# Kernel optimization log

Measured on AMD Instinct MI355X. Metric: run time of the kernel, lower is better.

## Reference

```python
import jax, jax.numpy as jnp
import numpy as np

N, E = 50000, 1600000
F_IN, EDGE_DIM, HID, HEADS, NCLS = 64, 16, 128, 4, 40
C = HID // HEADS  # per-head dim = 32


def setup_inputs() -> dict:
    key = jax.random.key(0)
    ks = jax.random.split(key, 20)
    s = 0.1
    inp = {
        'x': jax.random.normal(ks[0], (N, F_IN), jnp.float32),
        'edge_index': jax.random.randint(ks[1], (2, E), 0, N, jnp.int64),
        'edge_attr': jax.random.normal(ks[2], (E, EDGE_DIM), jnp.float32),
        # layer 1 params
        'W1': jax.random.normal(ks[3], (HID, F_IN), jnp.float32) * s,
        'as1': jax.random.normal(ks[4], (HEADS, C), jnp.float32) * s,
        'ad1': jax.random.normal(ks[5], (HEADS, C), jnp.float32) * s,
        'ae1': jax.random.normal(ks[6], (HEADS, C), jnp.float32) * s,
        'We1': jax.random.normal(ks[7], (HID, EDGE_DIM), jnp.float32) * s,
        'b1': jnp.zeros((HID,), jnp.float32),
        # layer 2 params
        'W2': jax.random.normal(ks[8], (HID, HID), jnp.float32) * s,
        'as2': jax.random.normal(ks[9], (HEADS, C), jnp.float32) * s,
        'ad2': jax.random.normal(ks[10], (HEADS, C), jnp.float32) * s,
        'ae2': jax.random.normal(ks[11], (HEADS, C), jnp.float32) * s,
        'We2': jax.random.normal(ks[12], (HID, EDGE_DIM), jnp.float32) * s,
        'b2': jnp.zeros((HID,), jnp.float32),
        # final classifier
        'Wlin': jax.random.normal(ks[13], (NCLS, HID), jnp.float32) * s,
        'blin': jnp.zeros((NCLS,), jnp.float32),
    }
    return inp


def gat_conv(x, src, dst, eattr, W, a_s, a_d, a_e, We, b):
    """PyG GATConv (concat=True, add_self_loops=True, fill_value='mean'), eval mode."""
    n = x.shape[0]
    H, Cd = a_s.shape
    h = (x @ W.T).reshape(n, H, Cd)  # [N,H,C]
    # self-loop edge_attr = per-destination mean of incoming edge_attr
    cnt = jax.ops.segment_sum(jnp.ones((dst.shape[0],), eattr.dtype), dst, num_segments=n)
    mean_ea = jax.ops.segment_sum(eattr, dst, num_segments=n) / jnp.maximum(cnt, 1.0)[:, None]
    loops = jnp.arange(n, dtype=src.dtype)
    s_idx = jnp.concatenate([src, loops])
    d_idx = jnp.concatenate([dst, loops])
    ea = jnp.concatenate([eattr, mean_ea], axis=0)  # [E+N, edge_dim]
    e = (ea @ We.T).reshape(-1, H, Cd)
    # edge-wise attention logits
    alpha = (h * a_s).sum(-1)[s_idx] + (h * a_d).sum(-1)[d_idx] + (e * a_e).sum(-1)  # [E+N,H]
    alpha = jax.nn.leaky_relu(alpha, 0.2)
    # segment softmax over destination neighborhoods (every node has a self-loop)
    amax = jax.ops.segment_max(alpha, d_idx, num_segments=n)
    ex = jnp.exp(alpha - amax[d_idx])
    den = jax.ops.segment_sum(ex, d_idx, num_segments=n)
    coef = ex / (den[d_idx] + 1e-16)
    out = jax.ops.segment_sum(h[s_idx] * coef[:, :, None], d_idx, num_segments=n)
    return out.reshape(n, H * Cd) + b


def reference(x, edge_index, edge_attr, W1, as1, ad1, ae1, We1, b1,
              W2, as2, ad2, ae2, We2, b2, Wlin, blin):
    src, dst = edge_index[0], edge_index[1]
    h = jax.nn.relu(gat_conv(x, src, dst, edge_attr, W1, as1, ad1, ae1, We1, b1))
    h = jax.nn.relu(gat_conv(h, src, dst, edge_attr, W2, as2, ad2, ae2, We2, b2))
    logits = h @ Wlin.T + blin
    return jax.nn.log_softmax(logits, axis=1)
```

## Files before the change

kernel.cpp:

```cpp
#include <hip/hip_runtime.h>
#include <hip/hip_bf16.h>
#include <math.h>


#define CHUNK 8192
#define CAPC 12288

typedef __attribute__((ext_vector_type(8))) short short8;
typedef __attribute__((ext_vector_type(4))) float floatx4;

__device__ __forceinline__ unsigned short f2bf(float f) {
  unsigned u = __float_as_uint(f);
  unsigned r = u + 0x7FFFu + ((u >> 16) & 1u);
  return (unsigned short)(r >> 16);
}
__device__ __forceinline__ float bf2f(unsigned short b) {
  return __uint_as_float(((unsigned)b) << 16);
}

__global__ __launch_bounds__(512) void hist_kernel(const int* __restrict__ dst,
                                                   int* __restrict__ bucketCnt,
                                                   int E, int NB) {
  __shared__ int hist[512];
  const int tid = threadIdx.x;
  hist[tid] = 0;
  __syncthreads();
  const int e0 = blockIdx.x * CHUNK, e1 = min(e0 + CHUNK, E);
  for (int e = e0 + tid; e < e1; e += 512) atomicAdd(&hist[dst[e] >> 7], 1);
  __syncthreads();
  if (tid < NB && hist[tid]) atomicAdd(&bucketCnt[tid], hist[tid]);
}

__global__ __launch_bounds__(512) void scanB_kernel(const int* __restrict__ bucketCnt,
                                                    int* __restrict__ bucketOffs,
                                                    int* __restrict__ bucketPos,
                                                    int* __restrict__ offs,
                                                    int NB, int N, int E) {
  __shared__ int sc[512];
  const int tid = threadIdx.x;
  const int v = (tid < NB) ? bucketCnt[tid] : 0;
  sc[tid] = v;
  __syncthreads();
  for (int off = 1; off < 512; off <<= 1) {
    int t = (tid >= off) ? sc[tid - off] : 0;
    __syncthreads();
    sc[tid] += t;
    __syncthreads();
  }
  const int excl = sc[tid] - v;
  if (tid < NB) { bucketOffs[tid] = excl; bucketPos[tid] = excl; }
  if (tid == 0) { bucketOffs[NB] = E; offs[N] = E; }
}

__global__ __launch_bounds__(512) void partB_kernel(const int* __restrict__ src,
                                                    const int* __restrict__ dst,
                                                    int* __restrict__ bucketPos,
                                                    int2* __restrict__ binned,
                                                    int E, int NB) {
  __shared__ int hist[512], sc[512], lbase[513], gbase[512], lcnt[512];
  __shared__ int2 stage[CHUNK];
  const int tid = threadIdx.x;
  const int e0 = blockIdx.x * CHUNK;
  const int e1 = min(e0 + CHUNK, E);
  hist[tid] = 0; lcnt[tid] = 0;
  __syncthreads();
  for (int e = e0 + tid; e < e1; e += 512) atomicAdd(&hist[dst[e] >> 7], 1);
  __syncthreads();
  sc[tid] = hist[tid];
  __syncthreads();
  for (int off = 1; off < 512; off <<= 1) {
    int t = (tid >= off) ? sc[tid - off] : 0;
    __syncthreads();
    sc[tid] += t;
    __syncthreads();
  }
  lbase[tid + 1] = sc[tid];
  if (tid == 0) lbase[0] = 0;
  if (tid < NB && hist[tid] > 0) gbase[tid] = atomicAdd(&bucketPos[tid], hist[tid]);
  __syncthreads();
  for (int e = e0 + tid; e < e1; e += 512) {
    const int d = dst[e];
    const int b = d >> 7;
    const int lr = atomicAdd(&lcnt[b], 1);
    int2 v;
    v.x = src[e];
    v.y = (int)(((unsigned)(d & 127) << 25) | (unsigned)e);
    stage[lbase[b] + lr] = v;
  }
  __syncthreads();
  const int total = e1 - e0;
  for (int t = tid; t < total; t += 512) {
    int lo = 0, hi = 511;
    while (lo < hi) {
      int mid = (lo + hi + 1) >> 1;
      if (lbase[mid] <= t) lo = mid; else hi = mid - 1;
    }
    binned[gbase[lo] + (t - lbase[lo])] = stage[t];
  }
}

__global__ __launch_bounds__(256) void passC_kernel(const int2* __restrict__ binned,
                                                    const int* __restrict__ bucketOffs,
                                                    int* __restrict__ srcS,
                                                    int* __restrict__ elist,
                                                    int* __restrict__ offs, int N) {
  __shared__ int cnt[128], dbase[129], dpos[128];
  __shared__ int2 stage[CAPC];
  const int tid = threadIdx.x;
  const int b = blockIdx.x;
  const int bo = bucketOffs[b], be = bucketOffs[b + 1];
  const int m = be - bo;
  if (tid < 128) { cnt[tid] = 0; dpos[tid] = 0; }
  __syncthreads();
  for (int t = tid; t < m; t += 256) {
    int2 v = binned[bo + t];
    if (t < CAPC) stage[t] = v;
    atomicAdd(&cnt[((unsigned)v.y) >> 25], 1);
  }
  __syncthreads();
  for (int off = 1; off < 128; off <<= 1) {
    int t = (tid < 128 && tid >= (unsigned)off) ? cnt[tid - off] : 0;
    __syncthreads();
    if (tid < 128) cnt[tid] += t;
    __syncthreads();
  }
  if (tid == 0) dbase[0] = 0;
  if (tid < 128) dbase[tid + 1] = cnt[tid];
  __syncthreads();
  const int dcnt = min(128, N - (b << 7));
  if (tid < dcnt) offs[(b << 7) + tid] = bo + dbase[tid];
  for (int t = tid; t < m; t += 256) {
    int2 v = (t < CAPC) ? stage[t] : binned[bo + t];
    const unsigned py = (unsigned)v.y;
    const int dl = py >> 25;
    const int p = dbase[dl] + atomicAdd(&dpos[dl], 1);
    srcS[bo + p] = v.x;
    elist[bo + p] = (int)(py & 0x1FFFFFFu);
  }
}

__global__ __launch_bounds__(128) void wa_kernel(const float* __restrict__ ae1,
                                                 const float* __restrict__ We1,
                                                 const float* __restrict__ ae2,
                                                 const float* __restrict__ We2,
                                                 float* __restrict__ Wa) {
  int t = threadIdx.x;
  const float* ae = (t < 64) ? ae1 : ae2;
  const float* We = (t < 64) ? We1 : We2;
  int h = (t >> 4) & 3;
  int d = t & 15;
  float s = 0.f;
  for (int c = 0; c < 32; ++c) s += ae[h * 32 + c] * We[(h * 32 + c) * 16 + d];
  Wa[t] = s;
}

__global__ __launch_bounds__(256) void cvt3_kernel(const float* __restrict__ a,
                                                   unsigned short* __restrict__ ao, int na,
                                                   const float* __restrict__ b,
                                                   unsigned short* __restrict__ bo, int nb,
                                                   const float* __restrict__ c,
                                                   unsigned short* __restrict__ co, int nc) {
  int i = blockIdx.x * 256 + threadIdx.x;
  if (i < na) ao[i] = f2bf(a[i]);
  else if (i < na + nb) bo[i - na] = f2bf(b[i - na]);
  else if (i < na + nb + nc) co[i - na - nb] = f2bf(c[i - na - nb]);
}

__global__ __launch_bounds__(256) void cvtw_kernel(const float* __restrict__ Wlin,
                                                   unsigned short* __restrict__ whi,
                                                   unsigned short* __restrict__ wlo) {
  int i = blockIdx.x * 256 + threadIdx.x;
  if (i >= 48 * 128) return;
  float v = (i < 40 * 128) ? Wlin[i] : 0.f;
  unsigned short h = f2bf(v);
  whi[i] = h;
  wlo[i] = f2bf(v - bf2f(h));
}

__global__ __launch_bounds__(256) void alphae12_kernel(const int* __restrict__ elist,
                                                       const float* __restrict__ ea,
                                                       const float* __restrict__ Wa,
                                                       unsigned short* __restrict__ ae1s,
                                                       unsigned short* __restrict__ ae2s,
                                                       int E) {
  __shared__ float wa[128];
  if (threadIdx.x < 128) wa[threadIdx.x] = Wa[threadIdx.x];
  __syncthreads();
  int j = blockIdx.x * 256 + threadIdx.x;
  if (j >= E) return;
  const int e = elist[j];
  const float4* p = (const float4*)(ea + (size_t)e * 16);
  float4 q0 = p[0], q1 = p[1], q2 = p[2], q3 = p[3];
  float v[16] = {q0.x, q0.y, q0.z, q0.w, q1.x, q1.y, q1.z, q1.w,
                 q2.x, q2.y, q2.z, q2.w, q3.x, q3.y, q3.z, q3.w};
  unsigned short rr[8];
#pragma unroll
  for (int h = 0; h < 8; ++h) {
    float s = 0.f;
#pragma unroll
    for (int d = 0; d < 16; ++d) s += v[d] * wa[h * 16 + d];
    rr[h] = f2bf(s);
  }
  ushort4 lo; lo.x = rr[0]; lo.y = rr[1]; lo.z = rr[2]; lo.w = rr[3];
  ushort4 hi; hi.x = rr[4]; hi.y = rr[5]; hi.z = rr[6]; hi.w = rr[7];
  *(ushort4*)(ae1s + (size_t)j * 4) = lo;
  *(ushort4*)(ae2s + (size_t)j * 4) = hi;
}

__global__ __launch_bounds__(256) void gemm_mfma_kernel(const unsigned short* __restrict__ X,
                                                        const unsigned short* __restrict__ Wb,
                                                        unsigned short* __restrict__ H,
                                                        int n, int K) {
  const int w = threadIdx.x >> 6;
  const int lane = threadIdx.x & 63;
  const int m0 = blockIdx.x * 64;
  const int quad = lane >> 4;
  const int l15 = lane & 15;
  floatx4 acc[4][2];
#pragma unroll
  for (int mt = 0; mt < 4; ++mt)
#pragma unroll
    for (int nt = 0; nt < 2; ++nt) acc[mt][nt] = (floatx4)(0.f);

  int rowm[4];
#pragma unroll
  for (int mt = 0; mt < 4; ++mt) {
    int r = m0 + mt * 16 + l15;
    rowm[mt] = (r < n) ? r : (n - 1);
  }
  const int ncol0 = (w << 5) + l15;

  for (int kc = 0; kc < K; kc += 32) {
    const int koff = kc + (quad << 3);
    short8 a[4], b[2];
#pragma unroll
    for (int mt = 0; mt < 4; ++mt)
      a[mt] = *(const short8*)(X + (size_t)rowm[mt] * K + koff);
#pragma unroll
    for (int nt = 0; nt < 2; ++nt)
      b[nt] = *(const short8*)(Wb + (size_t)(ncol0 + nt * 16) * K + koff);
#pragma unroll
    for (int mt = 0; mt < 4; ++mt)
#pragma unroll
      for (int nt = 0; nt < 2; ++nt)
        acc[mt][nt] = __builtin_amdgcn_mfma_f32_16x16x32_bf16(a[mt], b[nt], acc[mt][nt], 0, 0, 0);
  }
#pragma unroll
  for (int mt = 0; mt < 4; ++mt) {
    const int rbase = m0 + mt * 16 + (quad << 2);
#pragma unroll
    for (int nt = 0; nt < 2; ++nt) {
      const int col = ncol0 + nt * 16;
#pragma unroll
      for (int r = 0; r < 4; ++r) {
        const int row = rbase + r;
        if (row < n) H[(size_t)row * 128 + col] = f2bf(acc[mt][nt][r]);
      }
    }
  }
}

__global__ __launch_bounds__(256) void score_kernel(const unsigned short* __restrict__ h,
                                                    const float* __restrict__ a_s,
                                                    const float* __restrict__ a_d,
                                                    float* __restrict__ ssc,
                                                    float* __restrict__ dsc, int n) {
  int gid = blockIdx.x * 256 + threadIdx.x;
  int node = gid >> 6;
  int lane = threadIdx.x & 63;
  if (node >= n) return;
  int ch = lane * 2;
  ushort2 hq = *(const ushort2*)(h + (size_t)node * 128 + ch);
  float h0 = bf2f(hq.x), h1 = bf2f(hq.y);
  float ps = h0 * a_s[ch] + h1 * a_s[ch + 1];
  float pd = h0 * a_d[ch] + h1 * a_d[ch + 1];
#pragma unroll
  for (int off = 8; off; off >>= 1) {
    ps += __shfl_xor(ps, off, 16);
    pd += __shfl_xor(pd, off, 16);
  }
  if ((lane & 15) == 0) {
    int head = lane >> 4;
    ssc[node * 4 + head] = ps;
    dsc[node * 4 + head] = pd;
  }
}

__device__ __forceinline__ float leaky02(float a) { return a > 0.f ? a : 0.2f * a; }
__device__ __forceinline__ float sel4(float4 v, int h) {
  return (h == 0) ? v.x : (h == 1) ? v.y : (h == 2) ? v.z : v.w;
}

__global__ __launch_bounds__(256) void agg_kernel(const unsigned short* __restrict__ hin,
                                                  const float* __restrict__ ssc,
                                                  const float* __restrict__ dsc,
                                                  const unsigned short* __restrict__ aeS,
                                                  const int* __restrict__ offs,
                                                  const int* __restrict__ srcS,
                                                  const float* __restrict__ bias,
                                                  unsigned short* __restrict__ hout, int n) {
  __shared__ int sbuf[4][64];
  __shared__ float pbuf[4][256];
  const int tid = threadIdx.x;
  const int wv = tid >> 6;
  const int lane = tid & 63;
  const int node = blockIdx.x * 4 + wv;
  if (node >= n) return;
  const int l32 = lane & 31;
  const int half = lane >> 5;
  const int ch4 = l32 * 4;
  const int headB = l32 >> 3;
  const float4 dv = *(const float4*)(dsc + (size_t)node * 4);
  float4 l4 = make_float4(0.f, 0.f, 0.f, 0.f);
  float4 sa = make_float4(0.f, 0.f, 0.f, 0.f);
  float acc[4] = {0.f, 0.f, 0.f, 0.f};
  const int j0 = offs[node], j1 = offs[node + 1];

  for (int jc = j0; jc < j1; jc += 64) {
    const int len = min(64, j1 - jc);
    float4 p4 = make_float4(0.f, 0.f, 0.f, 0.f);
    int sv = 0;
    if (lane < len) {
      const int j = jc + lane;
      sv = srcS[j];
      const ushort4 aq = *(const ushort4*)(aeS + (size_t)j * 4);
      const float4 ae4 = make_float4(bf2f(aq.x), bf2f(aq.y), bf2f(aq.z), bf2f(aq.w));
      const float4 ss4 = *(const float4*)(ssc + (size_t)sv * 4);
      sa.x += ae4.x; sa.y += ae4.y; sa.z += ae4.z; sa.w += ae4.w;
      p4.x = __expf(leaky02(ss4.x + dv.x + ae4.x));
      p4.y = __expf(leaky02(ss4.y + dv.y + ae4.y));
      p4.z = __expf(leaky02(ss4.z + dv.z + ae4.z));
      p4.w = __expf(leaky02(ss4.w + dv.w + ae4.w));
    }
    sbuf[wv][lane] = sv;
    *(float4*)(&pbuf[wv][lane * 4]) = p4;
    l4.x += p4.x; l4.y += p4.y; l4.z += p4.z; l4.w += p4.w;
    int k = 0;
    for (; k + 8 <= len; k += 8) {
      int kk0 = k + half, kk1 = k + 2 + half, kk2 = k + 4 + half, kk3 = k + 6 + half;
      int s0 = sbuf[wv][kk0], s1 = sbuf[wv][kk1], s2 = sbuf[wv][kk2], s3 = sbuf[wv][kk3];
      float p0 = pbuf[wv][kk0 * 4 + headB], p1 = pbuf[wv][kk1 * 4 + headB];
      float p2 = pbuf[wv][kk2 * 4 + headB], p3 = pbuf[wv][kk3 * 4 + headB];
      uint2 d0 = *(const uint2*)(hin + (size_t)s0 * 128 + ch4);
      uint2 d1 = *(const uint2*)(hin + (size_t)s1 * 128 + ch4);
      uint2 d2 = *(const uint2*)(hin + (size_t)s2 * 128 + ch4);
      uint2 d3 = *(const uint2*)(hin + (size_t)s3 * 128 + ch4);
      acc[0] += p0 * __uint_as_float(d0.x << 16);
      acc[1] += p0 * __uint_as_float(d0.x & 0xFFFF0000u);
      acc[2] += p0 * __uint_as_float(d0.y << 16);
      acc[3] += p0 * __uint_as_float(d0.y & 0xFFFF0000u);
      acc[0] += p1 * __uint_as_float(d1.x << 16);
      acc[1] += p1 * __uint_as_float(d1.x & 0xFFFF0000u);
      acc[2] += p1 * __uint_as_float(d1.y << 16);
      acc[3] += p1 * __uint_as_float(d1.y & 0xFFFF0000u);
      acc[0] += p2 * __uint_as_float(d2.x << 16);
      acc[1] += p2 * __uint_as_float(d2.x & 0xFFFF0000u);
      acc[2] += p2 * __uint_as_float(d2.y << 16);
      acc[3] += p2 * __uint_as_float(d2.y & 0xFFFF0000u);
      acc[0] += p3 * __uint_as_float(d3.x << 16);
      acc[1] += p3 * __uint_as_float(d3.x & 0xFFFF0000u);
      acc[2] += p3 * __uint_as_float(d3.y << 16);
      acc[3] += p3 * __uint_as_float(d3.y & 0xFFFF0000u);
    }
    for (; k < len; k += 2) {
      int kk = k + half;
      if (kk < len) {
        int s = sbuf[wv][kk];
        float p = pbuf[wv][kk * 4 + headB];
        uint2 d = *(const uint2*)(hin + (size_t)s * 128 + ch4);
        acc[0] += p * __uint_as_float(d.x << 16);
        acc[1] += p * __uint_as_float(d.x & 0xFFFF0000u);
        acc[2] += p * __uint_as_float(d.y << 16);
        acc[3] += p * __uint_as_float(d.y & 0xFFFF0000u);
      }
    }
  }

#pragma unroll
  for (int off = 32; off; off >>= 1) {
    sa.x += __shfl_xor(sa.x, off);
    sa.y += __shfl_xor(sa.y, off);
    sa.z += __shfl_xor(sa.z, off);
    sa.w += __shfl_xor(sa.w, off);
    l4.x += __shfl_xor(l4.x, off);
    l4.y += __shfl_xor(l4.y, off);
    l4.z += __shfl_xor(l4.z, off);
    l4.w += __shfl_xor(l4.w, off);
  }
#pragma unroll
  for (int i = 0; i < 4; ++i) acc[i] += __shfl_xor(acc[i], 32);

  const int deg = j1 - j0;
  const float invd = 1.f / fmaxf((float)deg, 1.f);
  const float ssn = ssc[(size_t)node * 4 + headB];
  const float aloop = leaky02(ssn + sel4(dv, headB) + sel4(sa, headB) * invd);
  const float pl = __expf(aloop);
  const float lF = sel4(l4, headB) + pl;
  const uint2 hd = *(const uint2*)(hin + (size_t)node * 128 + ch4);
  const float hv0 = __uint_as_float(hd.x << 16);
  const float hv1 = __uint_as_float(hd.x & 0xFFFF0000u);
  const float hv2 = __uint_as_float(hd.y << 16);
  const float hv3 = __uint_as_float(hd.y & 0xFFFF0000u);
  const float inv = 1.f / (lF + 1e-16f);
  const float4 bi = *(const float4*)(bias + ch4);
  const float o0 = fmaxf((acc[0] + pl * hv0) * inv + bi.x, 0.f);
  const float o1 = fmaxf((acc[1] + pl * hv1) * inv + bi.y, 0.f);
  const float o2 = fmaxf((acc[2] + pl * hv2) * inv + bi.z, 0.f);
  const float o3 = fmaxf((acc[3] + pl * hv3) * inv + bi.w, 0.f);
  if (half == 0) {
    ushort4 o;
    o.x = f2bf(o0); o.y = f2bf(o1); o.z = f2bf(o2); o.w = f2bf(o3);
    *(ushort4*)(hout + (size_t)node * 128 + ch4) = o;
  }
}

__global__ __launch_bounds__(256) void classifier_kernel(const unsigned short* __restrict__ h,
                                                         const unsigned short* __restrict__ Whi,
                                                         const unsigned short* __restrict__ Wlo,
                                                         const float* __restrict__ blin,
                                                         float* __restrict__ out, int n) {
  const int w = threadIdx.x >> 6;
  const int lane = threadIdx.x & 63;
  const int quad = lane >> 4;
  const int l15 = lane & 15;
  const int row0 = blockIdx.x * 64 + w * 16;
  if (row0 >= n) return;
  int rowm = row0 + l15;
  if (rowm >= n) rowm = n - 1;
  floatx4 acc[3];
#pragma unroll
  for (int nt = 0; nt < 3; ++nt) acc[nt] = (floatx4)(0.f);
  const size_t hbase = (size_t)rowm * 128;
#pragma unroll
  for (int kc = 0; kc < 128; kc += 32) {
    const int koff = kc + (quad << 3);
    short8 a = *(const short8*)(h + hbase + koff);
#pragma unroll
    for (int nt = 0; nt < 3; ++nt) {
      short8 bh = *(const short8*)(Whi + (size_t)(nt * 16 + l15) * 128 + koff);
      short8 bl = *(const short8*)(Wlo + (size_t)(nt * 16 + l15) * 128 + koff);
      acc[nt] = __builtin_amdgcn_mfma_f32_16x16x32_bf16(a, bh, acc[nt], 0, 0, 0);
      acc[nt] = __builtin_amdgcn_mfma_f32_16x16x32_bf16(a, bl, acc[nt], 0, 0, 0);
    }
  }
  const float bl0 = blin[l15];
  const float bl1 = blin[16 + l15];
  const float bl2 = (l15 < 8) ? blin[32 + l15] : 0.f;
#pragma unroll
  for (int r = 0; r < 4; ++r) {
    const int rrow = row0 + (quad << 2) + r;
    const float v0 = acc[0][r] + bl0;
    const float v1 = acc[1][r] + bl1;
    const float v2 = (l15 < 8) ? (acc[2][r] + bl2) : -INFINITY;
    float m = fmaxf(v0, fmaxf(v1, v2));
#pragma unroll
    for (int off = 8; off; off >>= 1) m = fmaxf(m, __shfl_xor(m, off, 16));
    const float e2 = (l15 < 8) ? __expf(v2 - m) : 0.f;
    float s = __expf(v0 - m) + __expf(v1 - m) + e2;
#pragma unroll
    for (int off = 8; off; off >>= 1) s += __shfl_xor(s, off, 16);
    const float ls = m + __logf(s);
    if (rrow < n) {
      float* po = out + (size_t)rrow * 40;
      po[l15] = v0 - ls;
      po[16 + l15] = v1 - ls;
      if (l15 < 8) po[32 + l15] = v2 - ls;
    }
  }
}

extern "C" void kernel_launch(void* const* d_in, const int* in_sizes, int n_in,
                              void* d_out, int out_size, void* d_ws, size_t ws_size,
                              hipStream_t stream) {
  const float* x    = (const float*)d_in[0];
  const int*   eidx = (const int*)d_in[1];
  const float* ea   = (const float*)d_in[2];
  const float* W1   = (const float*)d_in[3];
  const float* as1  = (const float*)d_in[4];
  const float* ad1  = (const float*)d_in[5];
  const float* ae1w = (const float*)d_in[6];
  const float* We1  = (const float*)d_in[7];
  const float* b1   = (const float*)d_in[8];
  const float* W2   = (const float*)d_in[9];
  const float* as2  = (const float*)d_in[10];
  const float* ad2  = (const float*)d_in[11];
  const float* ae2w = (const float*)d_in[12];
  const float* We2  = (const float*)d_in[13];
  const float* b2   = (const float*)d_in[14];
  const float* Wlin = (const float*)d_in[15];
  const float* blin = (const float*)d_in[16];
  float* out = (float*)d_out;

  const int N = in_sizes[0] / 64;
  const int E = in_sizes[1] / 2;
  const int* src = eidx;
  const int* dst = eidx + E;
  const int NB = (N + 127) >> 7;

  char* wsb = (char*)d_ws;
  size_t off = 0;
  auto alloc = [&](size_t bytes) -> void* {
    void* p = wsb + off;
    off = (off + bytes + 255) & ~(size_t)255;
    return p;
  };
  int* bucketCnt  = (int*)alloc(512 * 4);
  int* bucketOffs = (int*)alloc(513 * 4);
  int* bucketPos  = (int*)alloc(512 * 4);
  int* offs       = (int*)alloc((size_t)(N + 1) * 4);
  void* bhA       = alloc((size_t)E * 8 > (size_t)N * 256 ? (size_t)E * 8 : (size_t)N * 256);
  int2* binned    = (int2*)bhA;
  unsigned short* hA = (unsigned short*)bhA;
  int* srcS       = (int*)alloc((size_t)E * 4);
  int* elist      = (int*)alloc((size_t)E * 4);
  float* Wa       = (float*)alloc(128 * 4);
  unsigned short* xb  = (unsigned short*)alloc((size_t)N * 64 * 2);
  unsigned short* Wb1 = (unsigned short*)alloc(128 * 64 * 2);
  unsigned short* Wb2 = (unsigned short*)alloc(128 * 128 * 2);
  unsigned short* Wlh = (unsigned short*)alloc(48 * 128 * 2);
  unsigned short* Wll = (unsigned short*)alloc(48 * 128 * 2);
  float* ssc      = (float*)alloc((size_t)N * 4 * 4);
  float* dsc      = (float*)alloc((size_t)N * 4 * 4);
  unsigned short* ae1s = (unsigned short*)alloc((size_t)E * 4 * 2);
  unsigned short* ae2s = (unsigned short*)alloc((size_t)E * 4 * 2);
  unsigned short* hB   = (unsigned short*)alloc((size_t)N * 128 * 2);

  const int ge = (E + 255) / 256;
  const int gg = (N + 63) / 64;
  const int gn = (N + 3) / 4;
  const int gp = (E + CHUNK - 1) / CHUNK;
  const int ncvt = N * 64 + 128 * 64 + 128 * 128;

  hipMemsetAsync(bucketCnt, 0, 512 * 4, stream);
  hist_kernel<<<gp, 512, 0, stream>>>(dst, bucketCnt, E, NB);
  scanB_kernel<<<1, 512, 0, stream>>>(bucketCnt, bucketOffs, bucketPos, offs, NB, N, E);
  partB_kernel<<<gp, 512, 0, stream>>>(src, dst, bucketPos, binned, E, NB);
  passC_kernel<<<NB, 256, 0, stream>>>(binned, bucketOffs, srcS, elist, offs, N);

  wa_kernel<<<1, 128, 0, stream>>>(ae1w, We1, ae2w, We2, Wa);
  cvt3_kernel<<<(ncvt + 255) / 256, 256, 0, stream>>>(x, xb, N * 64, W1, Wb1, 128 * 64,
                                                      W2, Wb2, 128 * 128);
  cvtw_kernel<<<24, 256, 0, stream>>>(Wlin, Wlh, Wll);
  alphae12_kernel<<<ge, 256, 0, stream>>>(elist, ea, Wa, ae1s, ae2s, E);

  gemm_mfma_kernel<<<gg, 256, 0, stream>>>(xb, Wb1, hA, N, 64);
  score_kernel<<<gn, 256, 0, stream>>>(hA, as1, ad1, ssc, dsc, N);
  agg_kernel<<<gn, 256, 0, stream>>>(hA, ssc, dsc, ae1s, offs, srcS, b1, hB, N);

  gemm_mfma_kernel<<<gg, 256, 0, stream>>>(hB, Wb2, hA, N, 128);
  score_kernel<<<gn, 256, 0, stream>>>(hA, as2, ad2, ssc, dsc, N);
  agg_kernel<<<gn, 256, 0, stream>>>(hA, ssc, dsc, ae2s, offs, srcS, b2, hB, N);

  classifier_kernel<<<gg, 256, 0, stream>>>(hB, Wlh, Wll, blin, out, N);
}
```

Before: 483.8 us.

## Map one aggregation node per half-wave with 8-deep unrolled neighbor gathers

The GAT aggregation kernel now assigns each destination node to 32 lanes instead of a full 64-lane wave, so each block covers 8 nodes. Edges are processed in 32-wide chunks, and the gather loop is unrolled 8-deep with all loads issued before any accumulation. This is meant to cut idle lanes for average-degree nodes, remove the cross-half accumulator reduction, and keep more memory loads in flight. The self-feature and bias loads are hoisted to the start of the kernel. In exchange, two nodes with different degrees now share one wave, which can cause loop divergence, and register pressure rises.

```diff
diff --git a/kernel.cpp b/kernel.cpp
--- a/kernel.cpp
+++ b/kernel.cpp
@@ -299,29 +299,29 @@
                                                   const int* __restrict__ srcS,
                                                   const float* __restrict__ bias,
                                                   unsigned short* __restrict__ hout, int n) {
-  __shared__ int sbuf[4][64];
-  __shared__ float pbuf[4][256];
+  __shared__ int sbuf[8][32];
+  __shared__ float pbuf[8][128];
   const int tid = threadIdx.x;
-  const int wv = tid >> 6;
-  const int lane = tid & 63;
-  const int node = blockIdx.x * 4 + wv;
+  const int hw = tid >> 5;
+  const int l32 = tid & 31;
+  const int node = blockIdx.x * 8 + hw;
   if (node >= n) return;
-  const int l32 = lane & 31;
-  const int half = lane >> 5;
   const int ch4 = l32 * 4;
   const int headB = l32 >> 3;
   const float4 dv = *(const float4*)(dsc + (size_t)node * 4);
+  const uint2 hd = *(const uint2*)(hin + (size_t)node * 128 + ch4);
+  const float4 bi = *(const float4*)(bias + ch4);
   float4 l4 = make_float4(0.f, 0.f, 0.f, 0.f);
   float4 sa = make_float4(0.f, 0.f, 0.f, 0.f);
   float acc[4] = {0.f, 0.f, 0.f, 0.f};
   const int j0 = offs[node], j1 = offs[node + 1];
 
-  for (int jc = j0; jc < j1; jc += 64) {
-    const int len = min(64, j1 - jc);
+  for (int jc = j0; jc < j1; jc += 32) {
+    const int len = min(32, j1 - jc);
     float4 p4 = make_float4(0.f, 0.f, 0.f, 0.f);
     int sv = 0;
-    if (lane < len) {
-      const int j = jc + lane;
+    if (l32 < len) {
+      const int j = jc + l32;
       sv = srcS[j];
       const ushort4 aq = *(const ushort4*)(aeS + (size_t)j * 4);
       const float4 ae4 = make_float4(bf2f(aq.x), bf2f(aq.y), bf2f(aq.z), bf2f(aq.w));
@@ -332,52 +332,44 @@
       p4.z = __expf(leaky02(ss4.z + dv.z + ae4.z));
       p4.w = __expf(leaky02(ss4.w + dv.w + ae4.w));
     }
-    sbuf[wv][lane] = sv;
-    *(float4*)(&pbuf[wv][lane * 4]) = p4;
+    sbuf[hw][l32] = sv;
+    *(float4*)(&pbuf[hw][l32 * 4]) = p4;
     l4.x += p4.x; l4.y += p4.y; l4.z += p4.z; l4.w += p4.w;
+
     int k = 0;
     for (; k + 8 <= len; k += 8) {
-      int kk0 = k + half, kk1 = k + 2 + half, kk2 = k + 4 + half, kk3 = k + 6 + half;
-      int s0 = sbuf[wv][kk0], s1 = sbuf[wv][kk1], s2 = sbuf[wv][kk2], s3 = sbuf[wv][kk3];
-      float p0 = pbuf[wv][kk0 * 4 + headB], p1 = pbuf[wv][kk1 * 4 + headB];
-      float p2 = pbuf[wv][kk2 * 4 + headB], p3 = pbuf[wv][kk3 * 4 + headB];
-      uint2 d0 = *(const uint2*)(hin + (size_t)s0 * 128 + ch4);
-      uint2 d1 = *(const uint2*)(hin + (size_t)s1 * 128 + ch4);
-      uint2 d2 = *(const uint2*)(hin + (size_t)s2 * 128 + ch4);
-      uint2 d3 = *(const uint2*)(hin + (size_t)s3 * 128 + ch4);
-      acc[0] += p0 * __uint_as_float(d0.x << 16);
-      acc[1] += p0 * __uint_as_float(d0.x & 0xFFFF0000u);
-      acc[2] += p0 * __uint_as_float(d0.y << 16);
-      acc[3] += p0 * __uint_as_float(d0.y & 0xFFFF0000u);
-      acc[0] += p1 * __uint_as_float(d1.x << 16);
-      acc[1] += p1 * __uint_as_float(d1.x & 0xFFFF0000u);
-      acc[2] += p1 * __uint_as_float(d1.y << 16);
-      acc[3] += p1 * __uint_as_float(d1.y & 0xFFFF0000u);
-      acc[0] += p2 * __uint_as_float(d2.x << 16);
-      acc[1] += p2 * __uint_as_float(d2.x & 0xFFFF0000u);
-      acc[2] += p2 * __uint_as_float(d2.y << 16);
-      acc[3] += p2 * __uint_as_float(d2.y & 0xFFFF0000u);
-      acc[0] += p3 * __uint_as_float(d3.x << 16);
-      acc[1] += p3 * __uint_as_float(d3.x & 0xFFFF0000u);
-      acc[2] += p3 * __uint_as_float(d3.y << 16);
-      acc[3] += p3 * __uint_as_float(d3.y & 0xFFFF0000u);
-    }
-    for (; k < len; k += 2) {
-      int kk = k + half;
-      if (kk < len) {
-        int s = sbuf[wv][kk];
-        float p = pbuf[wv][kk * 4 + headB];
-        uint2 d = *(const uint2*)(hin + (size_t)s * 128 + ch4);
-        acc[0] += p * __uint_as_float(d.x << 16);
-        acc[1] += p * __uint_as_float(d.x & 0xFFFF0000u);
-        acc[2] += p * __uint_as_float(d.y << 16);
-        acc[3] += p * __uint_as_float(d.y & 0xFFFF0000u);
+      int s[8];
+      float p[8];
+      uint2 d[8];
+#pragma unroll
+      for (int u = 0; u < 8; ++u) {
+        s[u] = sbuf[hw][k + u];
+        p[u] = pbuf[hw][(k + u) * 4 + headB];
       }
-    }
-  }
-
-#pragma unroll
-  for (int off = 32; off; off >>= 1) {
+#pragma unroll
+      for (int u = 0; u < 8; ++u)
+        d[u] = *(const uint2*)(hin + (size_t)s[u] * 128 + ch4);
+#pragma unroll
+      for (int u = 0; u < 8; ++u) {
+        acc[0] += p[u] * __uint_as_float(d[u].x << 16);
+        acc[1] += p[u] * __uint_as_float(d[u].x & 0xFFFF0000u);
+        acc[2] += p[u] * __uint_as_float(d[u].y << 16);
+        acc[3] += p[u] * __uint_as_float(d[u].y & 0xFFFF0000u);
+      }
+    }
+    for (; k < len; ++k) {
+      const int s = sbuf[hw][k];
+      const float p = pbuf[hw][k * 4 + headB];
+      const uint2 d = *(const uint2*)(hin + (size_t)s * 128 + ch4);
+      acc[0] += p * __uint_as_float(d.x << 16);
+      acc[1] += p * __uint_as_float(d.x & 0xFFFF0000u);
+      acc[2] += p * __uint_as_float(d.y << 16);
+      acc[3] += p * __uint_as_float(d.y & 0xFFFF0000u);
+    }
+  }
+
+#pragma unroll
+  for (int off = 16; off; off >>= 1) {
     sa.x += __shfl_xor(sa.x, off);
     sa.y += __shfl_xor(sa.y, off);
     sa.z += __shfl_xor(sa.z, off);
@@ -387,8 +379,6 @@
     l4.z += __shfl_xor(l4.z, off);
     l4.w += __shfl_xor(l4.w, off);
   }
-#pragma unroll
-  for (int i = 0; i < 4; ++i) acc[i] += __shfl_xor(acc[i], 32);
 
   const int deg = j1 - j0;
   const float invd = 1.f / fmaxf((float)deg, 1.f);
@@ -396,22 +386,18 @@
   const float aloop = leaky02(ssn + sel4(dv, headB) + sel4(sa, headB) * invd);
   const float pl = __expf(aloop);
   const float lF = sel4(l4, headB) + pl;
-  const uint2 hd = *(const uint2*)(hin + (size_t)node * 128 + ch4);
   const float hv0 = __uint_as_float(hd.x << 16);
   const float hv1 = __uint_as_float(hd.x & 0xFFFF0000u);
   const float hv2 = __uint_as_float(hd.y << 16);
   const float hv3 = __uint_as_float(hd.y & 0xFFFF0000u);
   const float inv = 1.f / (lF + 1e-16f);
-  const float4 bi = *(const float4*)(bias + ch4);
   const float o0 = fmaxf((acc[0] + pl * hv0) * inv + bi.x, 0.f);
   const float o1 = fmaxf((acc[1] + pl * hv1) * inv + bi.y, 0.f);
   const float o2 = fmaxf((acc[2] + pl * hv2) * inv + bi.z, 0.f);
   const float o3 = fmaxf((acc[3] + pl * hv3) * inv + bi.w, 0.f);
-  if (half == 0) {
-    ushort4 o;
-    o.x = f2bf(o0); o.y = f2bf(o1); o.z = f2bf(o2); o.w = f2bf(o3);
-    *(ushort4*)(hout + (size_t)node * 128 + ch4) = o;
-  }
+  ushort4 o;
+  o.x = f2bf(o0); o.y = f2bf(o1); o.z = f2bf(o2); o.w = f2bf(o3);
+  *(ushort4*)(hout + (size_t)node * 128 + ch4) = o;
 }
 
 __global__ __launch_bounds__(256) void classifier_kernel(const unsigned short* __restrict__ h,
@@ -527,7 +513,9 @@
 
   const int ge = (E + 255) / 256;
   const int gg = (N + 63) / 64;
-  const int gn = (N + 3) / 4;
+  const int gn = (N + 63) / 64;
+  const int gs = (N + 3) / 4;
+  const int ga = (N + 7) / 8;
   const int gp = (E + CHUNK - 1) / CHUNK;
   const int ncvt = N * 64 + 128 * 64 + 128 * 128;
 
@@ -544,12 +532,12 @@
   alphae12_kernel<<<ge, 256, 0, stream>>>(elist, ea, Wa, ae1s, ae2s, E);
 
   gemm_mfma_kernel<<<gg, 256, 0, stream>>>(xb, Wb1, hA, N, 64);
-  score_kernel<<<gn, 256, 0, stream>>>(hA, as1, ad1, ssc, dsc, N);
-  agg_kernel<<<gn, 256, 0, stream>>>(hA, ssc, dsc, ae1s, offs, srcS, b1, hB, N);
+  score_kernel<<<gs, 256, 0, stream>>>(hA, as1, ad1, ssc, dsc, N);
+  agg_kernel<<<ga, 256, 0, stream>>>(hA, ssc, dsc, ae1s, offs, srcS, b1, hB, N);
 
   gemm_mfma_kernel<<<gg, 256, 0, stream>>>(hB, Wb2, hA, N, 128);
-  score_kernel<<<gn, 256, 0, stream>>>(hA, as2, ad2, ssc, dsc, N);
-  agg_kernel<<<gn, 256, 0, stream>>>(hA, ssc, dsc, ae2s, offs, srcS, b2, hB, N);
+  score_kernel<<<gs, 256, 0, stream>>>(hA, as2, ad2, ssc, dsc, N);
+  agg_kernel<<<ga, 256, 0, stream>>>(hA, ssc, dsc, ae2s, offs, srcS, b2, hB, N);
 
   classifier_kernel<<<gg, 256, 0, stream>>>(hB, Wlh, Wll, blin, out, N);
 }
```

Result: no change. 492.9 us (+1.9%).
